# Kernel optimization log

Hardware: AMD Instinct MI355X
Metric: run time of the kernel (lower is better)

The kernel has to match this reference:

```python
import jax, jax.numpy as jnp
import numpy as np
import math
from jax import lax

SQRT_HALF = math.sqrt(0.5)

def _causal_dilated_conv(x, w, b, dilation):
    # x: [B, C, T], w: [O, I, K] (torch layout), causal left padding (K-1)*dilation
    k = w.shape[-1]
    pad = (k - 1) * dilation
    y = lax.conv_general_dilated(
        x, w,
        window_strides=(1,),
        padding=((pad, 0),),
        rhs_dilation=(dilation,),
        dimension_numbers=('NCH', 'OIH', 'NCH'),
    )
    return y + b[None, :, None]


def setup_inputs() -> dict:
    key = jax.random.key(0)
    ks = jax.random.split(key, 9)
    B, C, S, T, K = 8, 512, 256, 8192, 2
    scale = 1.0 / np.sqrt(C * K)
    return {
        'x': jax.random.normal(ks[0], (B, C, T), jnp.float32),
        'filter_w': jax.random.normal(ks[1], (C, C, K), jnp.float32) * scale,
        'filter_b': jax.random.normal(ks[2], (C,), jnp.float32) * scale,
        'gate_w': jax.random.normal(ks[3], (C, C, K), jnp.float32) * scale,
        'gate_b': jax.random.normal(ks[4], (C,), jnp.float32) * scale,
        'res_w': jax.random.normal(ks[5], (C, C), jnp.float32) / np.sqrt(C),
        'res_b': jax.random.normal(ks[6], (C,), jnp.float32) / np.sqrt(C),
        'skip_w': jax.random.normal(ks[7], (S, C), jnp.float32) / np.sqrt(C),
        'skip_b': jax.random.normal(ks[8], (S,), jnp.float32) / np.sqrt(C),
        'dilation': 4,
    }


def reference(x, filter_w, filter_b, gate_w, gate_b, res_w, res_b, skip_w, skip_b, dilation):
    filter_out = jnp.tanh(_causal_dilated_conv(x, filter_w, filter_b, dilation))
    gate_out = jax.nn.sigmoid(_causal_dilated_conv(x, gate_w, gate_b, dilation))
    x_gated = filter_out * gate_out  # [B, C, T]
    # 1x1 convs as channel contractions
    res_out = jnp.einsum('oc,bct->bot', res_w, x_gated) + res_b[None, :, None]
    skip_out = jnp.einsum('sc,bct->bst', skip_w, x_gated) + skip_b[None, :, None]
    return ((x + res_out) * SQRT_HALF, skip_out)
```

## Files before the change

### kernel.cpp

```cpp
#include <hip/hip_runtime.h>
#include <hip/hip_bf16.h>

typedef __attribute__((ext_vector_type(4))) float f32x4;
typedef __attribute__((ext_vector_type(8))) short bf16x8;
typedef __attribute__((ext_vector_type(4))) unsigned short u16x4;
typedef unsigned int   u32;
typedef unsigned short u16;

#define DPAD 8
#define B_   8
#define C_   512
#define T_   8192
#define S_   256

#define OFF_WBIG 0u
#define OFF_W2   2097152u
#define OFF_B1   2883584u
#define OFF_B2   2887680u
#define OFF_XT   2891776u
#define OFF_ZT   70066176u

__device__ __forceinline__ u16 f2bf(float f) {
  u32 u = __builtin_bit_cast(u32, f);
  u += 0x7FFFu + ((u >> 16) & 1u);
  return (u16)(u >> 16);
}
__device__ __forceinline__ float sigm_(float x) { return 1.0f / (1.0f + __expf(-x)); }
__device__ __forceinline__ float tanh_(float x) { return 2.0f / (1.0f + __expf(-2.0f * x)) - 1.0f; }

__device__ __forceinline__ void gload_lds16(const void* g, void* l) {
  __builtin_amdgcn_global_load_lds(
      (const __attribute__((address_space(1))) void*)g,
      (__attribute__((address_space(3))) void*)l, 16, 0, 0);
}

__global__ void pack_kernel(const float* __restrict__ fw, const float* __restrict__ fb,
                            const float* __restrict__ gw, const float* __restrict__ gb,
                            const float* __restrict__ rw, const float* __restrict__ rb,
                            const float* __restrict__ sw, const float* __restrict__ sb,
                            u16* __restrict__ Wbig, u16* __restrict__ W2,
                            float* __restrict__ b1, float* __restrict__ b2,
                            u16* __restrict__ Xt)
{
  int idx = blockIdx.x * 256 + threadIdx.x;
  if (idx < 1048576) {
    int row = idx >> 10, k = idx & 1023;
    int i = row >> 1;
    const float* src = (row & 1) ? gw : fw;
    float v = src[((i << 9) + (k & 511)) * 2 + ((k < 512) ? 1 : 0)];
    Wbig[idx] = f2bf(v);
    return;
  }
  idx -= 1048576;
  if (idx < 393216) {
    int r = idx >> 9, k = idx & 511;
    float v = (r < 512) ? rw[(r << 9) + k] : sw[((r - 512) << 9) + k];
    W2[idx] = f2bf(v);
    return;
  }
  idx -= 393216;
  if (idx < 1024) { b1[idx] = (idx & 1) ? gb[idx >> 1] : fb[idx >> 1]; return; }
  idx -= 1024;
  if (idx < 768) { b2[idx] = (idx < 512) ? rb[idx] : sb[idx - 512]; return; }
  idx -= 768;
  if (idx < B_ * DPAD * C_) {
    int b = idx >> 12;
    int rest = idx & 4095;
    Xt[(size_t)b * (T_ + DPAD) * C_ + rest] = 0;
  }
}

__global__ __launch_bounds__(256) void transpose_kernel(const float* __restrict__ x,
                                                        u16* __restrict__ Xt)
{
  __shared__ float tile[64][65];
  int bid = blockIdx.x;
  int ct = bid & 7, tt = (bid >> 3) & 127, b = bid >> 10;
  int w = threadIdx.x >> 6, ln = threadIdx.x & 63;
  const float* xp = x + ((size_t)(b * C_ + ct * 64)) * T_ + tt * 64;
#pragma unroll
  for (int r = 0; r < 16; ++r) {
    int cl = r * 4 + w;
    tile[cl][ln] = xp[(size_t)cl * T_ + ln];
  }
  __syncthreads();
  u16* op = Xt + ((size_t)b * (T_ + DPAD) + DPAD + tt * 64) * C_ + ct * 64;
  const int q = threadIdx.x & 15;
  const int cr = threadIdx.x >> 4;
#pragma unroll
  for (int r = 0; r < 4; ++r) {
    const int tl = r * 16 + cr;
    u16x4 v;
#pragma unroll
    for (int e = 0; e < 4; ++e) v[e] = f2bf(tile[q * 4 + e][tl]);
    *(u16x4*)(op + (size_t)tl * C_ + q * 4) = v;
  }
}

__global__ __launch_bounds__(512, 2) void gemm1_kernel(
    const u16* __restrict__ W, const u16* __restrict__ Xt,
    const float* __restrict__ b1, u16* __restrict__ Zt,
    const int* __restrict__ dptr)
{
  __shared__ __align__(16) u16 smem[65536];
  const int dcap = *dptr;
  const int tid = threadIdx.x;
  const int lane = tid & 63, wave = tid >> 6;
  const int wm = wave >> 2, wn = wave & 3;
  const int lp = lane & 15, lg = lane >> 4, lx = lane & 7;

  const int bid = blockIdx.x;
  const int xcd = bid & 7;
  const int idx = bid >> 3;
  const int mt  = idx & 3;
  const int nt  = (xcd << 5) | (idx >> 2);
  const int m0  = mt * 256;
  const int n0g = nt * 256;
  const int b = n0g >> 13, t0 = n0g & (T_ - 1);
  const size_t xtb = (size_t)b * (T_ + DPAD) * C_;

  const int srl = tid >> 3;
  const int skb = tid & 7;
  const int sxk = (skb ^ (srl & 7)) << 3;

  f32x4 acc[8][4];
#pragma unroll
  for (int i = 0; i < 8; ++i)
#pragma unroll
    for (int j = 0; j < 4; ++j) acc[i][j] = (f32x4){0.f, 0.f, 0.f, 0.f};

#define SQA(kt_, dd, q_) do {                                                  \
    const int row_ = (q_) * 64 + srl;                                          \
    gload_lds16(W + (size_t)(m0 + row_) * 1024 + (kt_) * 64 + sxk,             \
                smem + (dd) * 16384 + (q_) * 4096 + tid * 8);                  \
  } while (0)

#define SQB(kt_, dd, q_) do {                                                  \
    const int row_ = (q_) * 64 + srl;                                          \
    const int kg_  = (kt_) * 64 + sxk;                                         \
    const int rsh_ = (kg_ >= 512) ? dcap : 0;                                  \
    gload_lds16(Xt + xtb + (size_t)(DPAD + t0 + row_ - rsh_) * C_ + (kg_ & 511), \
                smem + 32768 + (dd) * 16384 + (q_) * 4096 + tid * 8);          \
  } while (0)

#define LDA_(Ab_, f_, kk_) \
  (*(const bf16x8*)((Ab_) + (size_t)(wm * 128 + (f_) * 16 + lp) * 64 + ((((kk_) * 4 + lg) ^ lx) << 3)))
#define LDB_(Bb_, j_, kk_) \
  (*(const bf16x8*)((Bb_) + (size_t)(wn * 64 + (j_) * 16 + lp) * 64 + ((((kk_) * 4 + lg) ^ lx) << 3)))

#define READA(a_, p_, Ab_) do {                                                \
    a_[0] = LDA_(Ab_, 2 * (p_), 0);  a_[1] = LDA_(Ab_, 2 * (p_), 1);           \
    a_[2] = LDA_(Ab_, 2 * (p_) + 1, 0); a_[3] = LDA_(Ab_, 2 * (p_) + 1, 1);    \
  } while (0)

#define MFMAPH(a_, p_) do {                                                    \
    __builtin_amdgcn_s_setprio(1);                                             \
    _Pragma("unroll") for (int kk_ = 0; kk_ < 2; ++kk_) {                      \
      _Pragma("unroll") for (int j_ = 0; j_ < 4; ++j_)                         \
        acc[2*(p_)][j_]   = __builtin_amdgcn_mfma_f32_16x16x32_bf16(a_[kk_],     bfr[j_][kk_], acc[2*(p_)][j_],   0, 0, 0); \
      _Pragma("unroll") for (int j_ = 0; j_ < 4; ++j_)                         \
        acc[2*(p_)+1][j_] = __builtin_amdgcn_mfma_f32_16x16x32_bf16(a_[2 + kk_], bfr[j_][kk_], acc[2*(p_)+1][j_], 0, 0, 0); \
    }                                                                          \
    __builtin_amdgcn_s_setprio(0);                                             \
  } while (0)

#define LGKM(n_) do { asm volatile("s_waitcnt lgkmcnt(" #n_ ")" ::: "memory"); \
                      __builtin_amdgcn_sched_barrier(0); } while (0)
#define VMW(n_)  do { asm volatile("s_waitcnt vmcnt(" #n_ ")" ::: "memory");   \
                      __builtin_amdgcn_sched_barrier(0); } while (0)

  bf16x8 bfr[4][2];
  bf16x8 aW[4], aX[4];

  SQB(0, 0, 0); SQB(0, 0, 1); SQB(0, 0, 2); SQB(0, 0, 3);
  SQA(0, 0, 0); SQA(0, 0, 1); SQA(0, 0, 2); SQA(0, 0, 3);
  VMW(0);
  __builtin_amdgcn_s_barrier();

  for (int t = 0; t < 15; ++t) {
    const int dd = t & 1, de = dd ^ 1;
    const u16* Ab = smem + dd * 16384;
    const u16* Bb = smem + 32768 + dd * 16384;
#pragma unroll
    for (int j = 0; j < 4; ++j) { bfr[j][0] = LDB_(Bb, j, 0); bfr[j][1] = LDB_(Bb, j, 1); }
    READA(aW, 0, Ab);
    READA(aX, 1, Ab);
    LGKM(4);
    MFMAPH(aW, 0);
    SQB(t + 1, de, 0); SQB(t + 1, de, 1); SQB(t + 1, de, 2); SQB(t + 1, de, 3);
    READA(aW, 2, Ab);
    LGKM(4);
    MFMAPH(aX, 1);
    SQA(t + 1, de, 0); SQA(t + 1, de, 1); SQA(t + 1, de, 2); SQA(t + 1, de, 3);
    READA(aX, 3, Ab);
    LGKM(4);
    MFMAPH(aW, 2);
    LGKM(0);
    MFMAPH(aX, 3);
    VMW(0);
    __builtin_amdgcn_s_barrier();
  }
  {
    const u16* Ab = smem + 16384;
    const u16* Bb = smem + 49152;
#pragma unroll
    for (int j = 0; j < 4; ++j) { bfr[j][0] = LDB_(Bb, j, 0); bfr[j][1] = LDB_(Bb, j, 1); }
    READA(aW, 0, Ab);
    READA(aX, 1, Ab);
    LGKM(4);
    MFMAPH(aW, 0);
    READA(aW, 2, Ab);
    LGKM(4);
    MFMAPH(aX, 1);
    READA(aX, 3, Ab);
    LGKM(4);
    MFMAPH(aW, 2);
    LGKM(0);
    MFMAPH(aX, 3);
  }

  __syncthreads();
  u16* const wt = smem + wave * 4608;
  const int g4 = lane >> 4, p = lane & 15;
#pragma unroll
  for (int i = 0; i < 8; ++i) {
    const int R = m0 + wm * 128 + i * 16 + (g4 << 2);
    const float bi0 = b1[R], bi1 = b1[R + 1], bi2 = b1[R + 2], bi3 = b1[R + 3];
    const int cl = i * 8 + g4 * 2;
#pragma unroll
    for (int j = 0; j < 4; ++j) {
      f32x4 v = acc[i][j];
      float z0 = tanh_(v[0] + bi0) * sigm_(v[1] + bi1);
      float z1 = tanh_(v[2] + bi2) * sigm_(v[3] + bi3);
      u32 pk = (u32)f2bf(z0) | ((u32)f2bf(z1) << 16);
      *(u32*)(wt + (j * 16 + p) * 72 + cl) = pk;
    }
  }
  const int cg = (m0 >> 1) + wm * 64 + (lane & 31) * 2;
  const int l5 = lane >> 5;
#pragma unroll
  for (int s = 0; s < 32; ++s) {
    const int tl = s * 2 + l5;
    u32 v = *(const u32*)(wt + tl * 72 + (lane & 31) * 2);
    *(u32*)(Zt + (size_t)(b * T_ + t0 + wn * 64 + tl) * C_ + cg) = v;
  }
#undef SQA
#undef SQB
#undef LDA_
#undef LDB_
#undef READA
#undef MFMAPH
#undef LGKM
#undef VMW
}

__global__ __launch_bounds__(256, 4) void gemm2_kernel(
    const u16* __restrict__ W2, const u16* __restrict__ Zt,
    const float* __restrict__ b2, const float* __restrict__ x,
    float* __restrict__ out)
{
  __shared__ __align__(16) u16 As[128 * 32];
  __shared__ __align__(16) u16 Bs[128 * 32];
  __shared__ __align__(16) float fstall[4 * 1088];
  const int tid = threadIdx.x;
  const int lane = tid & 63, wave = tid >> 6;
  const int wm = wave >> 1, wn = wave & 1;

  const int bid = blockIdx.x;
  const int xcd = bid & 7;
  const int idx = bid >> 3;
  const int mt  = idx % 6;
  const int nt  = (xcd << 6) + idx / 6;
  const int m0 = mt * 128;
  const int n0g = nt * 128;
  const int b = n0g >> 13, t0 = n0g & (T_ - 1);
  const int srow = tid >> 2;
  const int skk  = (tid & 3) * 8;

  f32x4 acc[4][4];
#pragma unroll
  for (int i = 0; i < 4; ++i)
#pragma unroll
    for (int j = 0; j < 4; ++j) acc[i][j] = (f32x4){0.f, 0.f, 0.f, 0.f};

  const int aoff = (wm * 64 + (lane & 15)) * 32 + (lane >> 4) * 8;
  const int boff = (wn * 64 + (lane & 15)) * 32 + (lane >> 4) * 8;
  const size_t ztb = (size_t)b * T_ * C_;

  for (int kc = 0; kc < 16; ++kc) {
    const int k = kc * 32 + skk;
    const u16* gA = W2 + (size_t)(m0 + srow) * 512 + k;
    const u16* gB = Zt + ztb + (size_t)(t0 + srow) * C_ + k;
    gload_lds16(gA,            As + tid * 8);
    gload_lds16(gA + 64 * 512, As + 2048 + tid * 8);
    gload_lds16(gB,            Bs + tid * 8);
    gload_lds16(gB + 64 * C_,  Bs + 2048 + tid * 8);
    asm volatile("s_waitcnt vmcnt(0)" ::: "memory");
    __syncthreads();
    bf16x8 af[4], bfr[4];
#pragma unroll
    for (int i = 0; i < 4; ++i) af[i]  = *(const bf16x8*)(As + aoff + i * 512);
#pragma unroll
    for (int j = 0; j < 4; ++j) bfr[j] = *(const bf16x8*)(Bs + boff + j * 512);
#pragma unroll
    for (int i = 0; i < 4; ++i)
#pragma unroll
      for (int j = 0; j < 4; ++j)
        acc[i][j] = __builtin_amdgcn_mfma_f32_16x16x32_bf16(af[i], bfr[j], acc[i][j], 0, 0, 0);
    __syncthreads();
  }

  float* const fst = fstall + wave * 1088;
  const int g = lane >> 4, p = lane & 15;
  const bool isres = (m0 < 512);

#pragma unroll
  for (int i = 0; i < 4; ++i) {
#pragma unroll
    for (int j = 0; j < 4; ++j)
#pragma unroll
      for (int r = 0; r < 4; ++r)
        fst[(g * 4 + r) * 68 + j * 16 + p] = acc[i][j][r];
#pragma unroll
    for (int q = 0; q < 4; ++q) {
      const int lrow = q * 4 + g;
      const int row = m0 + wm * 64 + i * 16 + lrow;
      const int t = t0 + wn * 64 + p * 4;
      f32x4 v = *(const f32x4*)&fst[lrow * 68 + p * 4];
      const float bias = b2[row];
      f32x4 res;
      if (isres) {
        const size_t o = ((size_t)(b * 512 + row)) * T_ + t;
        f32x4 xv = *(const f32x4*)(x + o);
#pragma unroll
        for (int e = 0; e < 4; ++e)
          res[e] = (xv[e] + v[e] + bias) * 0.70710678118654752f;
        *(f32x4*)(out + o) = res;
      } else {
        const size_t o = (size_t)33554432 + ((size_t)(b * 256 + (row - 512))) * T_ + t;
#pragma unroll
        for (int e = 0; e < 4; ++e)
          res[e] = v[e] + bias;
        *(f32x4*)(out + o) = res;
      }
    }
  }
}

extern "C" void kernel_launch(void* const* d_in, const int* in_sizes, int n_in,
                              void* d_out, int out_size, void* d_ws, size_t ws_size,
                              hipStream_t stream) {
  const float* x  = (const float*)d_in[0];
  const float* fw = (const float*)d_in[1];
  const float* fb = (const float*)d_in[2];
  const float* gw = (const float*)d_in[3];
  const float* gb = (const float*)d_in[4];
  const float* rw = (const float*)d_in[5];
  const float* rb = (const float*)d_in[6];
  const float* sw = (const float*)d_in[7];
  const float* sb = (const float*)d_in[8];
  const int* dil  = (const int*)d_in[9];

  char* ws = (char*)d_ws;
  u16*   Wbig = (u16*)(ws + OFF_WBIG);
  u16*   W2   = (u16*)(ws + OFF_W2);
  float* b1   = (float*)(ws + OFF_B1);
  float* b2   = (float*)(ws + OFF_B2);
  u16*   Xt   = (u16*)(ws + OFF_XT);
  u16*   Zt   = (u16*)(ws + OFF_ZT);
  float* out  = (float*)d_out;

  hipLaunchKernelGGL(pack_kernel, dim3(5767), dim3(256), 0, stream,
                     fw, fb, gw, gb, rw, rb, sw, sb, Wbig, W2, b1, b2, Xt);
  hipLaunchKernelGGL(transpose_kernel, dim3(8192), dim3(256), 0, stream, x, Xt);
  hipLaunchKernelGGL(gemm1_kernel, dim3(1024), dim3(512), 0, stream, Wbig, Xt, b1, Zt, dil);
  hipLaunchKernelGGL(gemm2_kernel, dim3(3072), dim3(256), 0, stream, W2, Zt, b2, x, out);
}
```

Measured before the change: 309.5 us.

## Double-buffer LDS in gemm2 and overlap next-tile loads with MFMA

Rewrites the gemm2 K-loop into a fully unrolled two-stage software pipeline. The next K-tile is issued into a second LDS buffer while MFMAs run on the current one, and one barrier per step replaces two. The A/B tiles and the epilogue staging area now share a single 32KB LDS array to keep the footprint down. The aim is to hide global-to-LDS latency in the second GEMM. The cost is more LDS pressure at 4 blocks per CU and priority tweaks via setprio.

```diff
diff --git a/kernel.cpp b/kernel.cpp
--- a/kernel.cpp
+++ b/kernel.cpp
@@ -259,9 +259,7 @@
     const float* __restrict__ b2, const float* __restrict__ x,
     float* __restrict__ out)
 {
-  __shared__ __align__(16) u16 As[128 * 32];
-  __shared__ __align__(16) u16 Bs[128 * 32];
-  __shared__ __align__(16) float fstall[4 * 1088];
+  __shared__ __align__(16) u16 smem2[16384];
   const int tid = threadIdx.x;
   const int lane = tid & 63, wave = tid >> 6;
   const int wm = wave >> 1, wn = wave & 1;
@@ -287,30 +285,76 @@
   const int boff = (wn * 64 + (lane & 15)) * 32 + (lane >> 4) * 8;
   const size_t ztb = (size_t)b * T_ * C_;
 
-  for (int kc = 0; kc < 16; ++kc) {
-    const int k = kc * 32 + skk;
-    const u16* gA = W2 + (size_t)(m0 + srow) * 512 + k;
-    const u16* gB = Zt + ztb + (size_t)(t0 + srow) * C_ + k;
-    gload_lds16(gA,            As + tid * 8);
-    gload_lds16(gA + 64 * 512, As + 2048 + tid * 8);
-    gload_lds16(gB,            Bs + tid * 8);
-    gload_lds16(gB + 64 * C_,  Bs + 2048 + tid * 8);
-    asm volatile("s_waitcnt vmcnt(0)" ::: "memory");
-    __syncthreads();
-    bf16x8 af[4], bfr[4];
-#pragma unroll
-    for (int i = 0; i < 4; ++i) af[i]  = *(const bf16x8*)(As + aoff + i * 512);
-#pragma unroll
-    for (int j = 0; j < 4; ++j) bfr[j] = *(const bf16x8*)(Bs + boff + j * 512);
-#pragma unroll
-    for (int i = 0; i < 4; ++i)
-#pragma unroll
-      for (int j = 0; j < 4; ++j)
-        acc[i][j] = __builtin_amdgcn_mfma_f32_16x16x32_bf16(af[i], bfr[j], acc[i][j], 0, 0, 0);
-    __syncthreads();
-  }
-
-  float* const fst = fstall + wave * 1088;
+  u16* const As0 = smem2;
+  u16* const As1 = smem2 + 4096;
+  u16* const Bs0 = smem2 + 8192;
+  u16* const Bs1 = smem2 + 12288;
+
+#define STAGE2(kc_, As_, Bs_) do {                                             \
+    const int k_ = (kc_) * 32 + skk;                                           \
+    gload_lds16(W2 + (size_t)(m0 + srow) * 512 + k_,           (As_) + tid * 8); \
+    gload_lds16(W2 + (size_t)(m0 + 64 + srow) * 512 + k_,      (As_) + 2048 + tid * 8); \
+    gload_lds16(Zt + ztb + (size_t)(t0 + srow) * C_ + k_,      (Bs_) + tid * 8); \
+    gload_lds16(Zt + ztb + (size_t)(t0 + 64 + srow) * C_ + k_, (Bs_) + 2048 + tid * 8); \
+  } while (0)
+
+#define LGKM0 do { asm volatile("s_waitcnt lgkmcnt(0)" ::: "memory");          \
+                   __builtin_amdgcn_sched_barrier(0); } while (0)
+#define VMW0  do { asm volatile("s_waitcnt vmcnt(0)" ::: "memory");            \
+                   __builtin_amdgcn_sched_barrier(0); } while (0)
+
+#define BODY2(kc_, Ac_, Bc_, An_, Bn_) do {                                    \
+    bf16x8 af_[4], bf_[4];                                                     \
+    _Pragma("unroll") for (int i_ = 0; i_ < 4; ++i_)                           \
+      af_[i_] = *(const bf16x8*)((Ac_) + aoff + i_ * 512);                     \
+    _Pragma("unroll") for (int j_ = 0; j_ < 4; ++j_)                           \
+      bf_[j_] = *(const bf16x8*)((Bc_) + boff + j_ * 512);                     \
+    STAGE2((kc_) + 1, An_, Bn_);                                               \
+    LGKM0;                                                                     \
+    __builtin_amdgcn_s_setprio(1);                                             \
+    _Pragma("unroll") for (int i_ = 0; i_ < 4; ++i_)                           \
+      _Pragma("unroll") for (int j_ = 0; j_ < 4; ++j_)                         \
+        acc[i_][j_] = __builtin_amdgcn_mfma_f32_16x16x32_bf16(af_[i_], bf_[j_], acc[i_][j_], 0, 0, 0); \
+    __builtin_amdgcn_s_setprio(0);                                             \
+    VMW0;                                                                      \
+    __builtin_amdgcn_s_barrier();                                              \
+  } while (0)
+
+  STAGE2(0, As0, Bs0);
+  VMW0;
+  __builtin_amdgcn_s_barrier();
+
+  BODY2(0,  As0, Bs0, As1, Bs1);
+  BODY2(1,  As1, Bs1, As0, Bs0);
+  BODY2(2,  As0, Bs0, As1, Bs1);
+  BODY2(3,  As1, Bs1, As0, Bs0);
+  BODY2(4,  As0, Bs0, As1, Bs1);
+  BODY2(5,  As1, Bs1, As0, Bs0);
+  BODY2(6,  As0, Bs0, As1, Bs1);
+  BODY2(7,  As1, Bs1, As0, Bs0);
+  BODY2(8,  As0, Bs0, As1, Bs1);
+  BODY2(9,  As1, Bs1, As0, Bs0);
+  BODY2(10, As0, Bs0, As1, Bs1);
+  BODY2(11, As1, Bs1, As0, Bs0);
+  BODY2(12, As0, Bs0, As1, Bs1);
+  BODY2(13, As1, Bs1, As0, Bs0);
+  BODY2(14, As0, Bs0, As1, Bs1);
+  {
+    bf16x8 af_[4], bf_[4];
+#pragma unroll
+    for (int i_ = 0; i_ < 4; ++i_) af_[i_] = *(const bf16x8*)(As1 + aoff + i_ * 512);
+#pragma unroll
+    for (int j_ = 0; j_ < 4; ++j_) bf_[j_] = *(const bf16x8*)(Bs1 + boff + j_ * 512);
+    LGKM0;
+#pragma unroll
+    for (int i_ = 0; i_ < 4; ++i_)
+#pragma unroll
+      for (int j_ = 0; j_ < 4; ++j_)
+        acc[i_][j_] = __builtin_amdgcn_mfma_f32_16x16x32_bf16(af_[i_], bf_[j_], acc[i_][j_], 0, 0, 0);
+  }
+
+  __syncthreads();
+  float* const fst = (float*)smem2 + wave * 1088;
   const int g = lane >> 4, p = lane & 15;
   const bool isres = (m0 < 512);
 
@@ -345,6 +389,10 @@
       }
     }
   }
+#undef STAGE2
+#undef LGKM0
+#undef VMW0
+#undef BODY2
 }
 
 extern "C" void kernel_launch(void* const* d_in, const int* in_sizes, int n_in,
```

After: 314.5 us. No clear change (+1.6%).
